# Performance work log

Measured on AMD Instinct MI355X. Metric: run time of the kernel, lower is better.

The kernel has to match this reference:

```python
import jax, jax.numpy as jnp
import numpy as np

B, C, H, W = 8, 320, 64, 64      # query feature map
S_KV, D_KV = 77, 1024            # key/value (text) tokens
HEADS, DIM_HEAD = 8, 64
INNER = HEADS * DIM_HEAD         # 512


def setup_inputs() -> dict:
    key = jax.random.key(0)
    ks = jax.random.split(key, 7)
    return {
        "query": jax.random.normal(ks[0], (B, C, H, W), dtype=jnp.float32),
        "key_value": jax.random.normal(ks[1], (B, S_KV, D_KV), dtype=jnp.float32),
        "Wq": jax.random.normal(ks[2], (C, INNER), dtype=jnp.float32) * (C ** -0.5),
        "Wk": jax.random.normal(ks[3], (D_KV, INNER), dtype=jnp.float32) * (D_KV ** -0.5),
        "Wv": jax.random.normal(ks[4], (D_KV, INNER), dtype=jnp.float32) * (D_KV ** -0.5),
        "Wo": jax.random.normal(ks[5], (INNER, C), dtype=jnp.float32) * (INNER ** -0.5),
        "bo": jnp.zeros((C,), dtype=jnp.float32),
    }


def reference(query, key_value, Wq, Wk, Wv, Wo, bo):
    b, c, h, w = query.shape
    n = h * w
    # [B,C,H,W] -> [B,N,C]
    q_flat = query.reshape(b, c, n).transpose(0, 2, 1)
    # projections, then split heads: [B, S, heads, dim_head]
    q = (q_flat @ Wq).reshape(b, n, HEADS, DIM_HEAD)
    k = (key_value @ Wk).reshape(b, S_KV, HEADS, DIM_HEAD)
    v = (key_value @ Wv).reshape(b, S_KV, HEADS, DIM_HEAD)
    scale = DIM_HEAD ** -0.5
    # attn logits: [B, heads, N, S_kv]
    logits = jnp.einsum('bnhd,bshd->bhns', q, k) * scale
    attn = jax.nn.softmax(logits, axis=-1)
    # weighted values -> merge heads: [B, N, inner]
    out = jnp.einsum('bhns,bshd->bnhd', attn, v).reshape(b, n, INNER)
    out = out @ Wo + bo  # dropout p=0.0 is identity
    # [B,N,C] -> [B,C,H,W]
    return out.transpose(0, 2, 1).reshape(b, c, h, w)
```

## Files before the change

kernel.cpp:

```cpp
#include <hip/hip_runtime.h>
#include <hip/hip_bf16.h>
#include <stdint.h>

#define BB     8
#define CC     320
#define NN     4096
#define SKV    77
#define HEADS  8
#define INNER  512
#define SCALE  0.125f

typedef float f32x4  __attribute__((ext_vector_type(4)));
typedef short bf16x8 __attribute__((ext_vector_type(8)));
typedef short s16x4  __attribute__((ext_vector_type(4)));

static __device__ __forceinline__ short f2bf(float f) {
  unsigned u = __float_as_uint(f);
  return (short)((u + 0x7fffu + ((u >> 16) & 1u)) >> 16);
}

static __device__ __forceinline__ void gll16(void* lds, const void* g) {
  auto gp = reinterpret_cast<const uint32_t __attribute__((address_space(1)))*>(
      reinterpret_cast<uintptr_t>(g));
  auto lp = reinterpret_cast<uint32_t __attribute__((address_space(3)))*>(
      reinterpret_cast<uintptr_t>(lds));
  __builtin_amdgcn_global_load_lds(gp, lp, 16, 0, 0);
}

__global__ __launch_bounds__(256) void prep_kernel(
    const float* __restrict__ kv, const float* __restrict__ Wk,
    const float* __restrict__ Wv, const float* __restrict__ Wq,
    const float* __restrict__ Wo, short* __restrict__ kv_bf,
    short* __restrict__ Wk_t, short* __restrict__ Wv_t,
    short* __restrict__ Wq_t, short* __restrict__ Wo_t,
    unsigned* __restrict__ zero_base) {
  __shared__ float T[64 * 65];
  const int blk = blockIdx.x, t = threadIdx.x;
  if (blk < 616) {
    const int base = blk * 1024;
    #pragma unroll
    for (int i = 0; i < 4; ++i) kv_bf[base + i*256 + t] = f2bf(kv[base + i*256 + t]);
    return;
  }
  if (blk >= 952) {
    const int base = (blk - 952) * 1024;
    #pragma unroll
    for (int i = 0; i < 4; ++i) zero_base[base + i*256 + t] = 0u;
    return;
  }
  const float* src; short* dst; int RS, CS, kt, ct; float scl = 1.0f;
  if (blk < 872) {
    const int tile = blk - 616;
    const bool isK = tile < 128;
    const int tt = isK ? tile : tile - 128;
    src = isK ? Wk : Wv; dst = isK ? Wk_t : Wv_t;
    RS = 1024; CS = 512; kt = tt >> 3; ct = tt & 7;
  } else if (blk < 912) {
    const int tt = blk - 872;
    src = Wq; dst = Wq_t; RS = 320; CS = 512; kt = tt >> 3; ct = tt & 7;
    scl = SCALE;
  } else {
    const int tt = blk - 912;
    src = Wo; dst = Wo_t; RS = 512; CS = 320; kt = tt / 5; ct = tt % 5;
  }
  const int cl = t & 63, rb = t >> 6;
  #pragma unroll
  for (int i = 0; i < 16; ++i)
    T[(rb + i*4)*65 + cl] = src[(size_t)(kt*64 + rb + i*4)*CS + ct*64 + cl];
  __syncthreads();
  #pragma unroll
  for (int i = 0; i < 16; ++i) {
    const int nl = rb + i*4;
    dst[(size_t)(ct*64 + nl)*RS + kt*64 + cl] = f2bf(T[cl*65 + nl] * scl);
  }
}

__global__ __launch_bounds__(256) void kvproj_kernel(
    const short* __restrict__ kv_bf, const short* __restrict__ Wk_t,
    const short* __restrict__ Wv_t, short* __restrict__ K_ws,
    short* __restrict__ V_ws) {
  const int t = threadIdx.x, w = t >> 6, lane = t & 63;
  const int l15 = lane & 15, q = lane >> 4;
  const int m0 = (blockIdx.x * 4 + w) * 16;
  const int y = blockIdx.y;
  const bool isK = (y < 8);
  const int h = y & 7;
  const short* __restrict__ Wt = isK ? Wk_t : Wv_t;
  const int arow = (m0 + l15 < 616) ? (m0 + l15) : 615;

  const f32x4 z = {0.f, 0.f, 0.f, 0.f};
  f32x4 acc[4] = {z, z, z, z};
  for (int k0 = 0; k0 < 1024; k0 += 32) {
    const bf16x8 a = *(const bf16x8*)(kv_bf + arow*1024 + k0 + q*8);
    #pragma unroll
    for (int nt = 0; nt < 4; ++nt) {
      const int n = h*64 + nt*16 + l15;
      const bf16x8 bfr = *(const bf16x8*)(Wt + n*1024 + k0 + q*8);
      acc[nt] = __builtin_amdgcn_mfma_f32_16x16x32_bf16(a, bfr, acc[nt], 0, 0, 0);
    }
  }
  #pragma unroll
  for (int nt = 0; nt < 4; ++nt) {
    const int d = nt*16 + l15;
    #pragma unroll
    for (int r = 0; r < 4; ++r) {
      const int row = m0 + q*4 + r;
      if (row < 616) {
        const int b = (int)(((unsigned)row * 54472u) >> 22);
        const int s = row - b*77;
        if (isK) K_ws[((b*8 + h)*80 + s)*64 + d] = f2bf(acc[nt][r]);
        else     V_ws[((b*8 + h)*64 + d)*96 + s] = f2bf(acc[nt][r]);
      }
    }
  }
}

__global__ __launch_bounds__(512, 2) void fused_kernel(
    const float* __restrict__ query, const short* __restrict__ Wq_t,
    const short* __restrict__ K_ws, const short* __restrict__ V_ws,
    const short* __restrict__ Wo_t, const float* __restrict__ bo,
    float* __restrict__ out) {
  const int t = threadIdx.x, w = t >> 6, lane = t & 63;
  const int l15 = lane & 15, q = lane >> 4;
  const int b = blockIdx.x >> 6;
  const int n0 = (blockIdx.x & 63) * 64;

  __shared__ short S[59904];

  const f32x4 z = {0.f, 0.f, 0.f, 0.f};

  {
    const float* qb = query + (size_t)b * CC * NN + n0;
    #pragma unroll
    for (int i = 0; i < 10; ++i) {
      const int f = i * 512 + t;
      const int c = f >> 4, n4 = (f & 15) * 4;
      const f32x4 v = *(const f32x4*)(qb + (size_t)c * NN + n4);
      #pragma unroll
      for (int j = 0; j < 4; ++j)
        S[(n4 + j) * 330 + c] = f2bf(v[j]);
    }
  }

  {
    f32x4 acc[4][4];
    #pragma unroll
    for (int mt = 0; mt < 4; ++mt)
      #pragma unroll
      for (int nt = 0; nt < 4; ++nt) acc[mt][nt] = z;

    auto stageB = [&](int it, int pbuf) {
      const int k0 = it * 32;
      short* dstb = S + 21120 + pbuf * 16384;
      #pragma unroll
      for (int p = 0; p < 4; ++p) {
        const int L = p * 512 + t;
        const int j = L >> 2, qp = L & 3;
        const int ql = qp ^ ((j >> 1) & 3);
        gll16(dstb + L * 8, Wq_t + (size_t)j * 320 + k0 + ql * 8);
      }
    };

    stageB(0, 0);
    __syncthreads();
    for (int it = 0; it < 10; ++it) {
      if (it + 1 < 10) stageB(it + 1, (it + 1) & 1);
      const int k0 = it * 32;
      const short* Bb = S + 21120 + (it & 1) * 16384;
      bf16x8 a[4], bb[4];
      #pragma unroll
      for (int mt = 0; mt < 4; ++mt)
        a[mt] = *(const bf16x8*)(S + (mt * 16 + l15) * 330 + k0 + q * 8);
      #pragma unroll
      for (int nt = 0; nt < 4; ++nt) {
        const int jr = w * 64 + nt * 16 + l15;
        const int a16 = jr * 4 + (q ^ ((jr >> 1) & 3));
        bb[nt] = *(const bf16x8*)(Bb + a16 * 8);
      }
      #pragma unroll
      for (int mt = 0; mt < 4; ++mt)
        #pragma unroll
        for (int nt = 0; nt < 4; ++nt)
          acc[mt][nt] = __builtin_amdgcn_mfma_f32_16x16x32_bf16(a[mt], bb[nt], acc[mt][nt], 0, 0, 0);
      __syncthreads();
    }
    #pragma unroll
    for (int mt = 0; mt < 4; ++mt)
      #pragma unroll
      for (int r = 0; r < 4; ++r) {
        const int tok = mt * 16 + q * 4 + r;
        #pragma unroll
        for (int nt = 0; nt < 4; ++nt)
          S[tok * 520 + w * 64 + nt * 16 + l15] = f2bf(acc[mt][nt][r]);
      }
  }

  {
    short* scrw = S + 33280 + w * 3328;
    #pragma unroll
    for (int i = 0; i < 4; ++i) {
      const int f = lane + i * 64;
      *(unsigned*)(scrw + (f >> 3) * 104 + 80 + (f & 7) * 2) = 0u;
    }
    const short* __restrict__ Kh = K_ws + (size_t)(b * 8 + w) * 80 * 64;
    const short* __restrict__ Vh = V_ws + (size_t)(b * 8 + w) * 64 * 96;

    for (int g = 0; g < 2; ++g) {
      const int tb = g * 32;
      f32x4 qk[2][5];
      #pragma unroll
      for (int nt = 0; nt < 2; ++nt)
        #pragma unroll
        for (int st = 0; st < 5; ++st) qk[nt][st] = z;
      #pragma unroll
      for (int f = 0; f < 2; ++f) {
        bf16x8 bq[2];
        #pragma unroll
        for (int nt = 0; nt < 2; ++nt)
          bq[nt] = *(const bf16x8*)(S + (tb + nt * 16 + l15) * 520 + w * 64 + f * 32 + q * 8);
        #pragma unroll
        for (int st = 0; st < 5; ++st) {
          const bf16x8 a = *(const bf16x8*)(Kh + (st * 16 + l15) * 64 + f * 32 + q * 8);
          #pragma unroll
          for (int nt = 0; nt < 2; ++nt)
            qk[nt][st] = __builtin_amdgcn_mfma_f32_16x16x32_bf16(a, bq[nt], qk[nt][st], 0, 0, 0);
        }
      }

      #pragma unroll
      for (int nt = 0; nt < 2; ++nt) {
        float mx = -1e30f;
        #pragma unroll
        for (int st = 0; st < 5; ++st)
          #pragma unroll
          for (int r = 0; r < 4; ++r) {
            const int s = st * 16 + q * 4 + r;
            const float vv = (s < SKV) ? qk[nt][st][r] : -1e30f;
            qk[nt][st][r] = vv;
            mx = fmaxf(mx, vv);
          }
        mx = fmaxf(mx, __shfl_xor(mx, 16));
        mx = fmaxf(mx, __shfl_xor(mx, 32));
        float sum = 0.f;
        #pragma unroll
        for (int st = 0; st < 5; ++st)
          #pragma unroll
          for (int r = 0; r < 4; ++r) {
            const int s = st * 16 + q * 4 + r;
            const float e = (s < SKV) ? __expf(qk[nt][st][r] - mx) : 0.f;
            qk[nt][st][r] = e;
            sum += e;
          }
        sum += __shfl_xor(sum, 16);
        sum += __shfl_xor(sum, 32);
        const float inv = 1.0f / sum;
        #pragma unroll
        for (int st = 0; st < 5; ++st) {
          s16x4 pv;
          #pragma unroll
          for (int r = 0; r < 4; ++r) pv[r] = f2bf(qk[nt][st][r] * inv);
          *(s16x4*)(scrw + (nt * 16 + l15) * 104 + st * 16 + q * 4) = pv;
        }
      }

      f32x4 ov[2][4];
      #pragma unroll
      for (int nt = 0; nt < 2; ++nt)
        #pragma unroll
        for (int dt = 0; dt < 4; ++dt) ov[nt][dt] = z;
      #pragma unroll
      for (int f = 0; f < 3; ++f) {
        bf16x8 bp[2];
        #pragma unroll
        for (int nt = 0; nt < 2; ++nt)
          bp[nt] = *(const bf16x8*)(scrw + (nt * 16 + l15) * 104 + f * 32 + q * 8);
        #pragma unroll
        for (int dt = 0; dt < 4; ++dt) {
          const bf16x8 a = *(const bf16x8*)(Vh + (dt * 16 + l15) * 96 + f * 32 + q * 8);
          #pragma unroll
          for (int nt = 0; nt < 2; ++nt)
            ov[nt][dt] = __builtin_amdgcn_mfma_f32_16x16x32_bf16(a, bp[nt], ov[nt][dt], 0, 0, 0);
        }
      }
      #pragma unroll
      for (int nt = 0; nt < 2; ++nt)
        #pragma unroll
        for (int dt = 0; dt < 4; ++dt) {
          s16x4 pv;
          #pragma unroll
          for (int r = 0; r < 4; ++r) pv[r] = f2bf(ov[nt][dt][r]);
          *(s16x4*)(S + (tb + nt * 16 + l15) * 520 + w * 64 + dt * 16 + q * 4) = pv;
        }
    }
  }
  __syncthreads();

  {
    const int wm = w & 3;
    const int wg = w >> 2;
    f32x4 oc[5][2];
    #pragma unroll
    for (int mt = 0; mt < 5; ++mt)
      #pragma unroll
      for (int nt = 0; nt < 2; ++nt) oc[mt][nt] = z;

    auto stageW = [&](int it, int pbuf) {
      const int k0 = it * 32;
      short* dstb = S + 33280 + pbuf * 10240;
      #pragma unroll
      for (int p = 0; p < 3; ++p) {
        const int L = p * 512 + t;
        if (L < 1280) {
          const int j = L >> 2, qp = L & 3;
          const int ql = qp ^ ((j >> 1) & 3);
          gll16(dstb + L * 8, Wo_t + (size_t)j * 512 + k0 + ql * 8);
        }
      }
    };

    stageW(0, 0);
    __syncthreads();
    for (int it = 0; it < 16; ++it) {
      if (it + 1 < 16) stageW(it + 1, (it + 1) & 1);
      const int k0 = it * 32;
      const short* Wb = S + 33280 + (it & 1) * 10240;
      bf16x8 a[5], bb[2];
      #pragma unroll
      for (int mt = 0; mt < 5; ++mt) {
        const int jr = wm * 80 + mt * 16 + l15;
        const int a16 = jr * 4 + (q ^ ((jr >> 1) & 3));
        a[mt] = *(const bf16x8*)(Wb + a16 * 8);
      }
      #pragma unroll
      for (int nt = 0; nt < 2; ++nt)
        bb[nt] = *(const bf16x8*)(S + (wg * 32 + nt * 16 + l15) * 520 + k0 + q * 8);
      #pragma unroll
      for (int mt = 0; mt < 5; ++mt)
        #pragma unroll
        for (int nt = 0; nt < 2; ++nt)
          oc[mt][nt] = __builtin_amdgcn_mfma_f32_16x16x32_bf16(a[mt], bb[nt], oc[mt][nt], 0, 0, 0);
      if (it + 1 < 16) __syncthreads();
    }
    #pragma unroll
    for (int mt = 0; mt < 5; ++mt)
      #pragma unroll
      for (int r = 0; r < 4; ++r) {
        const int c = wm * 80 + mt * 16 + q * 4 + r;
        const float bv = bo[c];
        float* rowp = out + ((size_t)(b * CC + c)) * NN + n0 + wg * 32;
        #pragma unroll
        for (int nt = 0; nt < 2; ++nt)
          rowp[nt * 16 + l15] = oc[mt][nt][r] + bv;
      }
  }
}

extern "C" void kernel_launch(void* const* d_in, const int* in_sizes, int n_in,
                              void* d_out, int out_size, void* d_ws, size_t ws_size,
                              hipStream_t stream) {
  const float* query = (const float*)d_in[0];
  const float* kv    = (const float*)d_in[1];
  const float* Wq    = (const float*)d_in[2];
  const float* Wk    = (const float*)d_in[3];
  const float* Wv    = (const float*)d_in[4];
  const float* Wo    = (const float*)d_in[5];
  const float* bo    = (const float*)d_in[6];
  float* out = (float*)d_out;

  char* p = (char*)d_ws;
  short* K_ws  = (short*)(p);
  short* V_ws  = (short*)(p +   819200);
  short* Wq_t  = (short*)(p +  1802240);
  short* Wo_t  = (short*)(p +  2129920);
  short* kv_bf = (short*)(p +  2457600);
  short* Wk_t  = (short*)(p +  3719168);
  short* Wv_t  = (short*)(p +  4767744);

  prep_kernel<<<1192, 256, 0, stream>>>(kv, Wk, Wv, Wq, Wo, kv_bf,
                                        Wk_t, Wv_t, Wq_t, Wo_t,
                                        (unsigned*)V_ws);
  kvproj_kernel<<<dim3(10, 16), 256, 0, stream>>>(kv_bf, Wk_t, Wv_t, K_ws, V_ws);
  fused_kernel<<<512, 512, 0, stream>>>(query, Wq_t, K_ws, V_ws, Wo_t, bo, out);
}
```

Measured before the change: 176.8 us.

## Give each wave private double-buffered weight staging to drop block barriers

The Q-projection and output-projection GEMM loops now stage weight tiles into per-wave LDS buffers. Each wave loads only the rows it consumes and waits with explicit vmcnt counts plus a scheduling barrier, which removes the per-iteration block-wide __syncthreads. The LDS footprint grows, and the launch-bounds occupancy hint is relaxed to give the compiler more registers. In exchange, the output projection loads some Wo tiles twice (two waves share the same rows), and correctness now depends on the hand-set waitcnt values and on wave-local ordering of the async LDS loads.

Result: no change. 175.5 us (-0.7%).

```diff
diff --git a/kernel.cpp b/kernel.cpp
--- a/kernel.cpp
+++ b/kernel.cpp
@@ -115,7 +115,7 @@
   }
 }
 
-__global__ __launch_bounds__(512, 2) void fused_kernel(
+__global__ __launch_bounds__(512) void fused_kernel(
     const float* __restrict__ query, const short* __restrict__ Wq_t,
     const short* __restrict__ K_ws, const short* __restrict__ V_ws,
     const short* __restrict__ Wo_t, const float* __restrict__ bo,
@@ -125,7 +125,7 @@
   const int b = blockIdx.x >> 6;
   const int n0 = (blockIdx.x & 63) * 64;
 
-  __shared__ short S[59904];
+  __shared__ short S[74240];
 
   const f32x4 z = {0.f, 0.f, 0.f, 0.f};
 
@@ -141,6 +141,7 @@
         S[(n4 + j) * 330 + c] = f2bf(v[j]);
     }
   }
+  __syncthreads();
 
   {
     f32x4 acc[4][4];
@@ -149,41 +150,49 @@
       #pragma unroll
       for (int nt = 0; nt < 4; ++nt) acc[mt][nt] = z;
 
-    auto stageB = [&](int it, int pbuf) {
+    short* W1w = S + 21120 + w * 4096;
+    const short* __restrict__ Wqw = Wq_t + (size_t)(w * 64) * 320;
+
+    auto stage1 = [&](int it, int pbuf) {
       const int k0 = it * 32;
-      short* dstb = S + 21120 + pbuf * 16384;
+      short* dstb = W1w + pbuf * 2048;
       #pragma unroll
       for (int p = 0; p < 4; ++p) {
-        const int L = p * 512 + t;
+        const int L = p * 64 + lane;
         const int j = L >> 2, qp = L & 3;
         const int ql = qp ^ ((j >> 1) & 3);
-        gll16(dstb + L * 8, Wq_t + (size_t)j * 320 + k0 + ql * 8);
+        gll16(dstb + L * 8, Wqw + (size_t)j * 320 + k0 + ql * 8);
       }
     };
 
-    stageB(0, 0);
-    __syncthreads();
+    stage1(0, 0);
     for (int it = 0; it < 10; ++it) {
-      if (it + 1 < 10) stageB(it + 1, (it + 1) & 1);
+      if (it + 1 < 10) {
+        stage1(it + 1, (it + 1) & 1);
+        asm volatile("s_waitcnt vmcnt(4)" ::: "memory");
+      } else {
+        asm volatile("s_waitcnt vmcnt(0)" ::: "memory");
+      }
+      __builtin_amdgcn_sched_barrier(0);
       const int k0 = it * 32;
-      const short* Bb = S + 21120 + (it & 1) * 16384;
+      const short* Bb = W1w + (it & 1) * 2048;
       bf16x8 a[4], bb[4];
       #pragma unroll
       for (int mt = 0; mt < 4; ++mt)
         a[mt] = *(const bf16x8*)(S + (mt * 16 + l15) * 330 + k0 + q * 8);
       #pragma unroll
       for (int nt = 0; nt < 4; ++nt) {
-        const int jr = w * 64 + nt * 16 + l15;
-        const int a16 = jr * 4 + (q ^ ((jr >> 1) & 3));
-        bb[nt] = *(const bf16x8*)(Bb + a16 * 8);
+        const int jr = nt * 16 + l15;
+        const int slot = jr * 4 + (q ^ ((jr >> 1) & 3));
+        bb[nt] = *(const bf16x8*)(Bb + slot * 8);
       }
       #pragma unroll
       for (int mt = 0; mt < 4; ++mt)
         #pragma unroll
         for (int nt = 0; nt < 4; ++nt)
           acc[mt][nt] = __builtin_amdgcn_mfma_f32_16x16x32_bf16(a[mt], bb[nt], acc[mt][nt], 0, 0, 0);
-      __syncthreads();
-    }
+    }
+    __syncthreads();
     #pragma unroll
     for (int mt = 0; mt < 4; ++mt)
       #pragma unroll
@@ -196,7 +205,7 @@
   }
 
   {
-    short* scrw = S + 33280 + w * 3328;
+    short* scrw = S + 33280 + w * 5120;
     #pragma unroll
     for (int i = 0; i < 4; ++i) {
       const int f = lane + i * 64;
@@ -304,32 +313,38 @@
       #pragma unroll
       for (int nt = 0; nt < 2; ++nt) oc[mt][nt] = z;
 
-    auto stageW = [&](int it, int pbuf) {
+    short* W3w = S + 33280 + w * 5120;
+    const short* __restrict__ Wow = Wo_t + (size_t)(wm * 80) * 512;
+
+    auto stage3 = [&](int it, int pbuf) {
       const int k0 = it * 32;
-      short* dstb = S + 33280 + pbuf * 10240;
-      #pragma unroll
-      for (int p = 0; p < 3; ++p) {
-        const int L = p * 512 + t;
-        if (L < 1280) {
-          const int j = L >> 2, qp = L & 3;
-          const int ql = qp ^ ((j >> 1) & 3);
-          gll16(dstb + L * 8, Wo_t + (size_t)j * 512 + k0 + ql * 8);
-        }
+      short* dstb = W3w + pbuf * 2560;
+      #pragma unroll
+      for (int p = 0; p < 5; ++p) {
+        const int L = p * 64 + lane;
+        const int j = L >> 2, qp = L & 3;
+        const int ql = qp ^ ((j >> 1) & 3);
+        gll16(dstb + L * 8, Wow + (size_t)j * 512 + k0 + ql * 8);
       }
     };
 
-    stageW(0, 0);
-    __syncthreads();
+    stage3(0, 0);
     for (int it = 0; it < 16; ++it) {
-      if (it + 1 < 16) stageW(it + 1, (it + 1) & 1);
+      if (it + 1 < 16) {
+        stage3(it + 1, (it + 1) & 1);
+        asm volatile("s_waitcnt vmcnt(5)" ::: "memory");
+      } else {
+        asm volatile("s_waitcnt vmcnt(0)" ::: "memory");
+      }
+      __builtin_amdgcn_sched_barrier(0);
       const int k0 = it * 32;
-      const short* Wb = S + 33280 + (it & 1) * 10240;
+      const short* Wb = W3w + (it & 1) * 2560;
       bf16x8 a[5], bb[2];
       #pragma unroll
       for (int mt = 0; mt < 5; ++mt) {
-        const int jr = wm * 80 + mt * 16 + l15;
-        const int a16 = jr * 4 + (q ^ ((jr >> 1) & 3));
-        a[mt] = *(const bf16x8*)(Wb + a16 * 8);
+        const int r = mt * 16 + l15;
+        const int slot = r * 4 + (q ^ ((r >> 1) & 3));
+        a[mt] = *(const bf16x8*)(Wb + slot * 8);
       }
       #pragma unroll
       for (int nt = 0; nt < 2; ++nt)
@@ -339,7 +354,6 @@
         #pragma unroll
         for (int nt = 0; nt < 2; ++nt)
           oc[mt][nt] = __builtin_amdgcn_mfma_f32_16x16x32_bf16(a[mt], bb[nt], oc[mt][nt], 0, 0, 0);
-      if (it + 1 < 16) __syncthreads();
     }
     #pragma unroll
     for (int mt = 0; mt < 5; ++mt)
```
